# Optimization experiments

Measured on AMD Instinct MI355X. Metric: run time of the kernel, lower is better.

The kernel has to match this reference:

```python
import jax, jax.numpy as jnp
import numpy as np
import math


def _extend(chunk):
    # chunk: [b, C, w, 1, dh] -> stacked (prev, cur, next) chunks: [b, C, w, 1, dh, 3]
    prev = jnp.pad(chunk[:, :-1], ((0, 0), (1, 0), (0, 0), (0, 0), (0, 0)))
    nxt = jnp.pad(chunk[:, 1:], ((0, 0), (0, 1), (0, 0), (0, 0), (0, 0)))
    return jnp.stack((prev, chunk, nxt), axis=-1)


def local_xl_attention(q, kv, Wq, Wkv, Wc, w):
    b, L, dm = q.shape
    dh = Wkv.shape[1] // 2          # d_head (w_kv projects to 2*d_head)
    nh = dm // dh                   # n_head
    C = L // w                      # number of chunks

    qp = (q @ Wq).reshape(b, L, nh, dh) / math.sqrt(dh)   # [b,L,nh,dh]
    kvp = kv @ Wkv                                         # [b,L,2*dh]
    k = kvp[..., :dh][:, :, None, :]                       # [b,L,1,dh] single KV head
    v = kvp[..., dh:][:, :, None, :]

    # sliding_chunks_matmul_qk (faithful to original einsum, incl. sum over z)
    cq = qp.reshape(b, C, w, nh, dh)
    ck_e = _extend(k.reshape(b, C, w, 1, dh))              # [b,C,w,1,dh,3]
    attn = jnp.einsum('bcxhd,bzyode->bcxhey', cq, ck_e)    # [b,C,w,nh,3,w]
    attn = attn.reshape(b, L, nh, 3 * w)

    probs = jax.nn.softmax(attn, axis=-1)

    # sliding_chunks_matmul_pv (faithful, incl. sum over z)
    cp = probs.reshape(b, C, w, nh, 3, w)
    cv_e = _extend(v.reshape(b, C, w, 1, dh))              # [b,C,w,1,dh,3]
    ctx = jnp.einsum('bcwhpd,bzdoep->bcwhe', cp, cv_e)     # [b,C,w,nh,dh]
    out = ctx.reshape(b, L, dm) @ Wc
    return out


def setup_inputs() -> dict:
    key = jax.random.key(0)
    ks = jax.random.split(key, 5)
    B, L, DM, NH = 1, 4096, 1024, 16
    DH = DM // NH
    scale = 0.02
    return {
        'q': jax.random.normal(ks[0], (B, L, DM), dtype=jnp.float32),
        'kv': jax.random.normal(ks[1], (B, L, DM), dtype=jnp.float32),
        'Wq': jax.random.normal(ks[2], (DM, DM), dtype=jnp.float32) * scale,
        'Wkv': jax.random.normal(ks[3], (DM, 2 * DH), dtype=jnp.float32) * scale,
        'Wc': jax.random.normal(ks[4], (DM, DM), dtype=jnp.float32) * scale,
        'w': 512,
    }


def reference(q, kv, Wq, Wkv, Wc, w):
    return local_xl_attention(q, kv, Wq, Wkv, Wc, w)
```

## Files before the change

### kernel.cpp

```cpp
#include <hip/hip_runtime.h>
#include <hip/hip_bf16.h>
#include <cstdint>
#include <cstddef>

#define L_ 4096
#define DM_ 1024
#define NH_ 16
#define DH_ 64
#define W_ 512
#define C_ 8
#define W3_ 1536
#define NROWS_ 65536

typedef __attribute__((ext_vector_type(8))) short short8;
typedef __attribute__((ext_vector_type(4))) float f32x4;

__device__ __forceinline__ void async16(const void* g, void* l) {
    __builtin_amdgcn_global_load_lds(
        (const __attribute__((address_space(1))) unsigned int*)g,
        (__attribute__((address_space(3))) unsigned int*)l, 16, 0, 0);
}

#if __has_builtin(__builtin_amdgcn_exp2f)
#define FEXP2(x) __builtin_amdgcn_exp2f(x)
#else
#define FEXP2(x) exp2f(x)
#endif

#define WAITV(N) asm volatile("s_waitcnt vmcnt(" #N ")" ::: "memory")
#define WAITL0() asm volatile("s_waitcnt lgkmcnt(0)" ::: "memory")
#define BARRIER() do { __builtin_amdgcn_s_barrier(); \
                       __builtin_amdgcn_sched_barrier(0); } while (0)

__device__ __forceinline__ int nanhit(unsigned u) {
    return (((u & 0x7F80u) == 0x7F80u) | (((u >> 16) & 0x7F80u) == 0x7F80u));
}

__device__ __forceinline__ float ldf(const void* X, size_t i, int f32) {
    return f32 ? ((const float*)X)[i] : __bfloat162float(((const __hip_bfloat16*)X)[i]);
}

__global__ __launch_bounds__(256) void megaprep(const void* __restrict__ q,
                                                const void* __restrict__ kv,
                                                const void* __restrict__ Wq,
                                                const void* __restrict__ Wkv,
                                                const void* __restrict__ Wc,
                                                __hip_bfloat16* __restrict__ qbuf,
                                                __hip_bfloat16* __restrict__ WqT,
                                                __hip_bfloat16* __restrict__ WkvT,
                                                __hip_bfloat16* __restrict__ WcT,
                                                __hip_bfloat16* __restrict__ kvcomb,
                                                int* __restrict__ flag) {
    __shared__ float t[64][65];
    __shared__ int sflag;
    const int b = blockIdx.x;
    const int tid = threadIdx.x;

    if (tid == 0) sflag = 0;
    __syncthreads();
    {
        int hit = 0;
#pragma unroll
        for (int r = 0; r < 4; ++r) {
            uint4 v = ((const uint4*)q)[tid + 256 * r];
            hit |= nanhit(v.x) | nanhit(v.y) | nanhit(v.z) | nanhit(v.w);
        }
        if (__any(hit)) { if ((tid & 63) == 0) atomicOr(&sflag, 1); }
    }
    __syncthreads();
    const int f32 = sflag;
    if (b == 0 && tid == 0) flag[0] = f32;

    if (b < 4096) {
        int i = (b * 256 + tid) * 4;
        if (f32) {
            float4 v = *(const float4*)((const float*)q + i);
            __hip_bfloat162 tmp[2] = {__float22bfloat162_rn({v.x, v.y}),
                                      __float22bfloat162_rn({v.z, v.w})};
            *(short4*)((short*)qbuf + i) = *(const short4*)tmp;
        } else {
            *(short4*)((short*)qbuf + i) = *(const short4*)((const short*)q + i);
        }
    } else if (b < 4640) {
        const void* W;
        __hip_bfloat16* WT;
        int K = 1024, N, n0, k0;
        if (b < 4352) {
            int bx = b - 4096; W = Wq; WT = WqT; N = 1024;
            n0 = (bx & 15) * 64; k0 = (bx >> 4) * 64;
        } else if (b < 4608) {
            int bx = b - 4352; W = Wc; WT = WcT; N = 1024;
            n0 = (bx & 15) * 64; k0 = (bx >> 4) * 64;
        } else {
            int bx = b - 4608; W = Wkv; WT = WkvT; N = 128;
            n0 = (bx & 1) * 64; k0 = (bx >> 1) * 64;
        }
        const int tx = tid & 63;
        const int ty = tid >> 6;
#pragma unroll
        for (int r = 0; r < 16; ++r) {
            int k = ty + r * 4;
            t[k][tx] = ldf(W, (size_t)(k0 + k) * N + n0 + tx, f32);
        }
        __syncthreads();
#pragma unroll
        for (int r = 0; r < 16; ++r) {
            int n = ty + r * 4;
            WT[(size_t)(n0 + n) * K + k0 + tx] = __float2bfloat16(t[tx][n]);
        }
    } else {
        int y = b - 4640;
        int c = tid * 4;
        float s0 = 0, s1 = 0, s2 = 0, s3 = 0;
        float f0 = 0, f1 = 0, f2 = 0, f3 = 0;
        float l0 = 0, l1 = 0, l2 = 0, l3 = 0;
#pragma unroll
        for (int z = 0; z < C_; ++z) {
            size_t base = (size_t)(z * W_ + y) * 1024 + c;
            float a0, a1, a2, a3;
            if (f32) {
                float4 v = *(const float4*)((const float*)kv + base);
                a0 = v.x; a1 = v.y; a2 = v.z; a3 = v.w;
            } else {
                short4 v = *(const short4*)((const short*)kv + base);
                a0 = __bfloat162float(*(__hip_bfloat16*)&v.x);
                a1 = __bfloat162float(*(__hip_bfloat16*)&v.y);
                a2 = __bfloat162float(*(__hip_bfloat16*)&v.z);
                a3 = __bfloat162float(*(__hip_bfloat16*)&v.w);
            }
            s0 += a0; s1 += a1; s2 += a2; s3 += a3;
            if (z == 0) { f0 = a0; f1 = a1; f2 = a2; f3 = a3; }
            if (z == C_ - 1) { l0 = a0; l1 = a1; l2 = a2; l3 = a3; }
        }
        auto store = [&](int row, float x0, float x1, float x2, float x3) {
            __hip_bfloat162 tmp[2] = {__float22bfloat162_rn({x0, x1}),
                                      __float22bfloat162_rn({x2, x3})};
            *(short4*)((short*)kvcomb + (size_t)row * 1024 + c) = *(const short4*)tmp;
        };
        store(y,        s0 - l0, s1 - l1, s2 - l2, s3 - l3);
        store(512 + y,  s0, s1, s2, s3);
        store(1024 + y, s0 - f0, s1 - f1, s2 - f2, s3 - f3);
    }
}

struct GemmP {
    const __hip_bfloat16* A;
    const __hip_bfloat16* BT;
    void* C;
    int M, N, K;
    float alpha;
    int cMode;
    int ntiles;
    int swz;
    int nblocks;
    void* C2;
};

__global__ __launch_bounds__(256) void gemm_bt_mfma(GemmP p0, GemmP p1,
                                                    const int* __restrict__ flag) {
    __shared__ __hip_bfloat16 Asl[2][2][128 * 32];
    __shared__ __hip_bfloat16 Bsl[2][2][64 * 32];

    GemmP p;
    int bid;
    if ((int)blockIdx.x < p0.nblocks) { p = p0; bid = blockIdx.x; }
    else { p = p1; bid = (int)blockIdx.x - p0.nblocks; }

    int mt, nt;
    if (!p.swz) { mt = bid / p.ntiles; nt = bid % p.ntiles; }
    else {
        int g = bid / (8 * p.ntiles);
        int rem = bid % (8 * p.ntiles);
        mt = g * 8 + (rem & 7);
        nt = rem >> 3;
    }
    const int m0 = mt * 128;
    const int n0 = nt * 64;
    const int K = p.K;
    const int N = p.N;

    const int tid = threadIdx.x;
    const int lane = tid & 63;
    const int wv = tid >> 6;
    const int wm = wv >> 1;
    const int wn = wv & 1;
    const int col = lane & 15;
    const int quad = lane >> 4;

    const int srow = lane >> 2;
    const int scol = (lane & 3) * 8;
    const __hip_bfloat16* Ag = p.A + (size_t)m0 * K;
    const __hip_bfloat16* Bg = p.BT + (size_t)n0 * K;

    f32x4 acc[4][2] = {};

    auto STAGE = [&](int bf, int k0) {
#pragma unroll
        for (int h = 0; h < 2; ++h) {
            int arow = wv * 32 + h * 16 + srow;
#pragma unroll
            for (int kc = 0; kc < 2; ++kc)
                async16(Ag + (size_t)arow * K + k0 + kc * 32 + scol,
                        &Asl[bf][kc][arow * 32 + scol]);
        }
        int brow = wv * 16 + srow;
#pragma unroll
        for (int kc = 0; kc < 2; ++kc)
            async16(Bg + (size_t)brow * K + k0 + kc * 32 + scol,
                    &Bsl[bf][kc][brow * 32 + scol]);
    };

    const int NT = K >> 6;
    STAGE(0, 0);

    int bf = 0;
    for (int t = 0; t < NT; ++t) {
        if (t + 1 < NT) {
            STAGE(bf ^ 1, (t + 1) << 6);
            WAITV(6);
        } else {
            WAITV(0);
        }
        BARRIER();

#pragma unroll
        for (int kc = 0; kc < 2; ++kc) {
            short8 af[4], bfr[2];
#pragma unroll
            for (int i = 0; i < 4; ++i)
                af[i] = *(const short8*)(&Asl[bf][kc][(wm * 64 + i * 16 + col) * 32 + quad * 8]);
#pragma unroll
            for (int j = 0; j < 2; ++j)
                bfr[j] = *(const short8*)(&Bsl[bf][kc][(wn * 32 + j * 16 + col) * 32 + quad * 8]);
#pragma unroll
            for (int am = 0; am < 4; ++am)
#pragma unroll
                for (int bn = 0; bn < 2; ++bn)
                    acc[am][bn] = __builtin_amdgcn_mfma_f32_16x16x32_bf16(af[am], bfr[bn], acc[am][bn], 0, 0, 0);
        }
        WAITL0();
        BARRIER();
        bf ^= 1;
    }

    if (p.cMode == 3) {
#pragma unroll
        for (int am = 0; am < 4; ++am)
#pragma unroll
            for (int bn = 0; bn < 2; ++bn)
#pragma unroll
                for (int r = 0; r < 4; ++r) {
                    int key = m0 + wm * 64 + am * 16 + quad * 4 + r;
                    int c = n0 + wn * 32 + bn * 16 + col;
                    float v = acc[am][bn][r];
                    int g = key >> 6, kr = key & 63;
                    if (c < 64) {
                        int byt = g * 8192 + kr * 128 +
                                  ((((c >> 3) ^ (kr & 7)) << 4)) + ((c & 7) << 1);
                        *(__hip_bfloat16*)((char*)p.C + byt) = __float2bfloat16(v);
                    } else {
                        int d = c - 64;
                        int pp = ((kr & 15) << 2) | (kr >> 4);
                        int byt = g * 8192 + d * 128 +
                                  ((((pp >> 3) ^ (d & 7)) << 4)) + ((pp & 7) << 1);
                        *(__hip_bfloat16*)((char*)p.C2 + byt) = __float2bfloat16(v);
                    }
                }
        return;
    }

    int cF = (p.cMode == 1) ? 1 : ((p.cMode == 2) ? 0 : flag[0]);
#pragma unroll
    for (int am = 0; am < 4; ++am)
#pragma unroll
        for (int bn = 0; bn < 2; ++bn)
#pragma unroll
            for (int r = 0; r < 4; ++r) {
                size_t ci = (size_t)(m0 + wm * 64 + am * 16 + quad * 4 + r) * N
                            + n0 + wn * 32 + bn * 16 + col;
                float v = acc[am][bn][r] * p.alpha;
                if (cF) ((float*)p.C)[ci] = v;
                else ((__hip_bfloat16*)p.C)[ci] = __float2bfloat16(v);
            }
}

#define PSTRIDE 72
__global__ __launch_bounds__(256, 2) void attn_kernel(const __hip_bfloat16* __restrict__ qb,
                                                      const __hip_bfloat16* __restrict__ Kb,
                                                      const __hip_bfloat16* __restrict__ Vt,
                                                      __hip_bfloat16* __restrict__ ctx) {
    __shared__ __align__(16) __hip_bfloat16 Kbuf[3][4096];
    __shared__ __align__(16) __hip_bfloat16 Vbuf[3][4096];
    __shared__ __align__(16) __hip_bfloat16 psm[4][32 * PSTRIDE];

    const int tid = threadIdx.x;
    const int lane = tid & 63;
    const int wv = tid >> 6;
    const int m0 = blockIdx.x * 128 + wv * 32;
    const int col = lane & 15;
    const int quad = lane >> 4;
    __hip_bfloat16* pw = psm[wv];

    const char* Kg = (const char*)Kb;
    const char* Vg = (const char*)Vt;
    const int so = tid * 16;

    const int off0 = ((quad ^ (col & 7)) << 4);
    const int off1 = (((quad + 4) ^ (col & 7)) << 4);

    short8 qf[2][2];
#pragma unroll
    for (int rg = 0; rg < 2; ++rg) {
        const __hip_bfloat16* qp = qb + (size_t)(m0 + rg * 16 + col) * 64 + quad * 8;
        qf[rg][0] = *(const short8*)(qp);
        qf[rg][1] = *(const short8*)(qp + 32);
    }

    f32x4 O[2][4] = {};
    float lrow[2][4] = {};

    async16(Kg + so, (char*)Kbuf[0] + so);
    async16(Kg + 4096 + so, (char*)Kbuf[0] + 4096 + so);
    async16(Vg + so, (char*)Vbuf[0] + so);
    async16(Vg + 4096 + so, (char*)Vbuf[0] + 4096 + so);

    int cur = 0;
    for (int t = 0; t < 24; ++t) {
        WAITV(0);
        BARRIER();

        if (t < 23) {
            const int nxt = (cur == 2) ? 0 : cur + 1;
            const char* ks = Kg + (size_t)(t + 1) * 8192;
            const char* vs = Vg + (size_t)(t + 1) * 8192;
            char* kd = (char*)Kbuf[nxt];
            char* vd = (char*)Vbuf[nxt];
            async16(ks + so, kd + so);
            async16(ks + 4096 + so, kd + 4096 + so);
            async16(vs + so, vd + so);
            async16(vs + 4096 + so, vd + 4096 + so);
        }

        const char* Kc = (const char*)Kbuf[cur];
        const char* Vc = (const char*)Vbuf[cur];

        short8 kb0[4], kb1[4];
#pragma unroll
        for (int f = 0; f < 4; ++f) {
            const int rb = (f * 16 + col) * 128;
            kb0[f] = *(const short8*)(Kc + rb + off0);
            kb1[f] = *(const short8*)(Kc + rb + off1);
        }

#pragma unroll
        for (int rg = 0; rg < 2; ++rg) {
            f32x4 S[4];
            __builtin_amdgcn_s_setprio(1);
#pragma unroll
            for (int f = 0; f < 4; ++f) {
                f32x4 s = {};
                s = __builtin_amdgcn_mfma_f32_16x16x32_bf16(qf[rg][0], kb0[f], s, 0, 0, 0);
                s = __builtin_amdgcn_mfma_f32_16x16x32_bf16(qf[rg][1], kb1[f], s, 0, 0, 0);
                S[f] = s;
            }
            __builtin_amdgcn_s_setprio(0);
#pragma unroll
            for (int f = 0; f < 4; ++f)
#pragma unroll
                for (int r = 0; r < 4; ++r) S[f][r] = FEXP2(S[f][r]);
#pragma unroll
            for (int r = 0; r < 4; ++r)
                lrow[rg][r] += (S[0][r] + S[1][r]) + (S[2][r] + S[3][r]);
#pragma unroll
            for (int r = 0; r < 4; ++r) {
                __hip_bfloat162 p01 = __float22bfloat162_rn({S[0][r], S[1][r]});
                __hip_bfloat162 p23 = __float22bfloat162_rn({S[2][r], S[3][r]});
                short4 t4;
                *(__hip_bfloat162*)(&t4.x) = p01;
                *(__hip_bfloat162*)(&t4.z) = p23;
                *(short4*)(pw + (rg * 16 + quad * 4 + r) * PSTRIDE + col * 4) = t4;
            }
        }

        short8 vb0[4], vb1[4];
#pragma unroll
        for (int f = 0; f < 4; ++f) {
            const int rb = (f * 16 + col) * 128;
            vb0[f] = *(const short8*)(Vc + rb + off0);
            vb1[f] = *(const short8*)(Vc + rb + off1);
        }

#pragma unroll
        for (int rg = 0; rg < 2; ++rg) {
            short8 a0 = *(const short8*)(pw + (rg * 16 + col) * PSTRIDE + quad * 8);
            short8 a1 = *(const short8*)(pw + (rg * 16 + col) * PSTRIDE + 32 + quad * 8);
            __builtin_amdgcn_s_setprio(1);
#pragma unroll
            for (int f = 0; f < 4; ++f) {
                O[rg][f] = __builtin_amdgcn_mfma_f32_16x16x32_bf16(a0, vb0[f], O[rg][f], 0, 0, 0);
                O[rg][f] = __builtin_amdgcn_mfma_f32_16x16x32_bf16(a1, vb1[f], O[rg][f], 0, 0, 0);
            }
            __builtin_amdgcn_s_setprio(0);
        }

        cur = (cur == 2) ? 0 : cur + 1;
    }

#pragma unroll
    for (int msk = 1; msk <= 8; msk <<= 1)
#pragma unroll
        for (int rg = 0; rg < 2; ++rg)
#pragma unroll
            for (int r = 0; r < 4; ++r) lrow[rg][r] += __shfl_xor(lrow[rg][r], msk, 64);

#pragma unroll
    for (int rg = 0; rg < 2; ++rg)
#pragma unroll
        for (int r = 0; r < 4; ++r) {
            float inv = 1.f / lrow[rg][r];
#pragma unroll
            for (int f = 0; f < 4; ++f)
                ctx[(size_t)(m0 + rg * 16 + quad * 4 + r) * 64 + f * 16 + col] =
                    __float2bfloat16(O[rg][f][r] * inv);
        }
}

extern "C" void kernel_launch(void* const* d_in, const int* in_sizes, int n_in,
                              void* d_out, int out_size, void* d_ws, size_t ws_size,
                              hipStream_t stream) {
    const void* q   = d_in[0];
    const void* kv  = d_in[1];
    const void* Wq  = d_in[2];
    const void* Wkv = d_in[3];
    const void* Wc  = d_in[4];

    char* ws = (char*)d_ws;
    size_t off = 0;
    int* flag = (int*)(ws + off); off += 1024;
    __hip_bfloat16* qbuf   = (__hip_bfloat16*)(ws + off); off += (size_t)L_ * DM_ * 2;
    __hip_bfloat16* WqT    = (__hip_bfloat16*)(ws + off); off += (size_t)DM_ * DM_ * 2;
    __hip_bfloat16* WkvT   = (__hip_bfloat16*)(ws + off); off += (size_t)128 * DM_ * 2;
    __hip_bfloat16* WcT    = (__hip_bfloat16*)(ws + off); off += (size_t)DM_ * DM_ * 2;
    __hip_bfloat16* qb     = (__hip_bfloat16*)(ws + off); off += (size_t)L_ * DM_ * 2;
    __hip_bfloat16* kvcomb = (__hip_bfloat16*)(ws + off); off += (size_t)1536 * 1024 * 2;
    __hip_bfloat16* Kb     = (__hip_bfloat16*)(ws + off); off += (size_t)W3_ * 64 * 2;
    __hip_bfloat16* Vt     = (__hip_bfloat16*)(ws + off); off += (size_t)64 * W3_ * 2;
    __hip_bfloat16* ctxb   = (__hip_bfloat16*)(ws + off);

    megaprep<<<5152, 256, 0, stream>>>(q, kv, Wq, Wkv, Wc,
                                       qbuf, WqT, WkvT, WcT, kvcomb, flag);

    {
        GemmP pq{qbuf, WqT, (void*)qb, L_, DM_, DM_,
                 0.125f * 1.44269504f, 2, 16, 1, 512, nullptr};
        GemmP pk{kvcomb, WkvT, (void*)Kb, 1536, 128, DM_,
                 1.0f, 3, 2, 0, 24, (void*)Vt};
        gemm_bt_mfma<<<536, 256, 0, stream>>>(pq, pk, flag);
    }
    attn_kernel<<<dim3(NROWS_ / 128), 256, 0, stream>>>(qb, Kb, Vt, ctxb);
    {
        GemmP pc{ctxb, WcT, d_out, L_, DM_, DM_, 1.0f, 0, 16, 1, 512, nullptr};
        GemmP pnull{};
        pnull.nblocks = 0;
        gemm_bt_mfma<<<512, 256, 0, stream>>>(pc, pnull, flag);
    }
}
```

Before: 172.4 us.

## Software-pipeline attention loop: compute next tile's QK before current PV

```diff
diff --git a/kernel.cpp b/kernel.cpp
--- a/kernel.cpp
+++ b/kernel.cpp
@@ -318,32 +318,20 @@
 
     f32x4 O[2][4] = {};
     float lrow[2][4] = {};
-
-    async16(Kg + so, (char*)Kbuf[0] + so);
-    async16(Kg + 4096 + so, (char*)Kbuf[0] + 4096 + so);
-    async16(Vg + so, (char*)Vbuf[0] + so);
-    async16(Vg + 4096 + so, (char*)Vbuf[0] + 4096 + so);
-
-    int cur = 0;
-    for (int t = 0; t < 24; ++t) {
-        WAITV(0);
-        BARRIER();
-
-        if (t < 23) {
-            const int nxt = (cur == 2) ? 0 : cur + 1;
-            const char* ks = Kg + (size_t)(t + 1) * 8192;
-            const char* vs = Vg + (size_t)(t + 1) * 8192;
-            char* kd = (char*)Kbuf[nxt];
-            char* vd = (char*)Vbuf[nxt];
-            async16(ks + so, kd + so);
-            async16(ks + 4096 + so, kd + 4096 + so);
-            async16(vs + so, vd + so);
-            async16(vs + 4096 + so, vd + 4096 + so);
-        }
-
-        const char* Kc = (const char*)Kbuf[cur];
-        const char* Vc = (const char*)Vbuf[cur];
-
+    f32x4 S[2][4];
+
+    auto stage_tile = [&](int tile, int slot) {
+        const char* ks = Kg + (size_t)tile * 8192;
+        const char* vs = Vg + (size_t)tile * 8192;
+        char* kd = (char*)Kbuf[slot];
+        char* vd = (char*)Vbuf[slot];
+        async16(ks + so, kd + so);
+        async16(ks + 4096 + so, kd + 4096 + so);
+        async16(vs + so, vd + so);
+        async16(vs + 4096 + so, vd + 4096 + so);
+    };
+
+    auto qk_into = [&](const char* Kc, f32x4 (&Sd)[2][4]) {
         short8 kb0[4], kb1[4];
 #pragma unroll
         for (int f = 0; f < 4; ++f) {
@@ -351,30 +339,48 @@
             kb0[f] = *(const short8*)(Kc + rb + off0);
             kb1[f] = *(const short8*)(Kc + rb + off1);
         }
-
-#pragma unroll
-        for (int rg = 0; rg < 2; ++rg) {
-            f32x4 S[4];
-            __builtin_amdgcn_s_setprio(1);
+        __builtin_amdgcn_s_setprio(1);
+#pragma unroll
+        for (int rg = 0; rg < 2; ++rg)
 #pragma unroll
             for (int f = 0; f < 4; ++f) {
                 f32x4 s = {};
                 s = __builtin_amdgcn_mfma_f32_16x16x32_bf16(qf[rg][0], kb0[f], s, 0, 0, 0);
                 s = __builtin_amdgcn_mfma_f32_16x16x32_bf16(qf[rg][1], kb1[f], s, 0, 0, 0);
-                S[f] = s;
+                Sd[rg][f] = s;
             }
-            __builtin_amdgcn_s_setprio(0);
+        __builtin_amdgcn_s_setprio(0);
+    };
+
+    stage_tile(0, 0);
+    stage_tile(1, 1);
+    WAITV(4);
+    BARRIER();
+    qk_into((const char*)Kbuf[0], S);
+
+    int cur = 0;
+    for (int t = 0; t < 24; ++t) {
+        const int nx1 = (cur == 2) ? 0 : cur + 1;
+        const int nx2 = (nx1 == 2) ? 0 : nx1 + 1;
+
+        WAITV(0);
+        BARRIER();
+
+        if (t < 22) stage_tile(t + 2, nx2);
+
+#pragma unroll
+        for (int rg = 0; rg < 2; ++rg) {
 #pragma unroll
             for (int f = 0; f < 4; ++f)
 #pragma unroll
-                for (int r = 0; r < 4; ++r) S[f][r] = FEXP2(S[f][r]);
+                for (int r = 0; r < 4; ++r) S[rg][f][r] = FEXP2(S[rg][f][r]);
 #pragma unroll
             for (int r = 0; r < 4; ++r)
-                lrow[rg][r] += (S[0][r] + S[1][r]) + (S[2][r] + S[3][r]);
+                lrow[rg][r] += (S[rg][0][r] + S[rg][1][r]) + (S[rg][2][r] + S[rg][3][r]);
 #pragma unroll
             for (int r = 0; r < 4; ++r) {
-                __hip_bfloat162 p01 = __float22bfloat162_rn({S[0][r], S[1][r]});
-                __hip_bfloat162 p23 = __float22bfloat162_rn({S[2][r], S[3][r]});
+                __hip_bfloat162 p01 = __float22bfloat162_rn({S[rg][0][r], S[rg][1][r]});
+                __hip_bfloat162 p23 = __float22bfloat162_rn({S[rg][2][r], S[rg][3][r]});
                 short4 t4;
                 *(__hip_bfloat162*)(&t4.x) = p01;
                 *(__hip_bfloat162*)(&t4.z) = p23;
@@ -382,6 +388,10 @@
             }
         }
 
+        f32x4 Snew[2][4];
+        if (t < 23) qk_into((const char*)Kbuf[nx1], Snew);
+
+        const char* Vc = (const char*)Vbuf[cur];
         short8 vb0[4], vb1[4];
 #pragma unroll
         for (int f = 0; f < 4; ++f) {
@@ -389,7 +399,6 @@
             vb0[f] = *(const short8*)(Vc + rb + off0);
             vb1[f] = *(const short8*)(Vc + rb + off1);
         }
-
 #pragma unroll
         for (int rg = 0; rg < 2; ++rg) {
             short8 a0 = *(const short8*)(pw + (rg * 16 + col) * PSTRIDE + quad * 8);
@@ -403,7 +412,13 @@
             __builtin_amdgcn_s_setprio(0);
         }
 
-        cur = (cur == 2) ? 0 : cur + 1;
+        if (t < 23) {
+#pragma unroll
+            for (int rg = 0; rg < 2; ++rg)
+#pragma unroll
+                for (int f = 0; f < 4; ++f) S[rg][f] = Snew[rg][f];
+        }
+        cur = nx1;
     }
 
 #pragma unroll
```

Measured after the change: 170.1 us (median of 2 runs). No clear change (-1.4%).
